# Optimization experiments

Measured on AMD Instinct MI355X. Metric: run time of the kernel, lower is better.

## Reference

```python
import jax, jax.numpy as jnp
import numpy as np

B, T, E, H, L, V = 2, 1024, 1024, 16, 4, 32000
HS = E // H
EPS = 1e-5


def layernorm(x, g, b):
    m = jnp.mean(x, axis=-1, keepdims=True)
    v = jnp.mean((x - m) ** 2, axis=-1, keepdims=True)
    return (x - m) * jax.lax.rsqrt(v + EPS) * g + b


def setup_inputs() -> dict:
    key = jax.random.key(0)
    ks = jax.random.split(key, 20)
    s = 0.02
    inp = {
        "ids": jax.random.randint(ks[0], (B, T), 0, V, dtype=jnp.int32),
        "emb": jax.random.normal(ks[1], (V, E), jnp.float32) * s,
        "pos": jax.random.normal(ks[2], (T, E), jnp.float32) * s,
        "wq": jax.random.normal(ks[3], (L, E, E), jnp.float32) * s,
        "bq": jnp.zeros((L, E), jnp.float32),
        "wk": jax.random.normal(ks[4], (L, E, E), jnp.float32) * s,
        "bk": jnp.zeros((L, E), jnp.float32),
        "wv": jax.random.normal(ks[5], (L, E, E), jnp.float32) * s,
        "bv": jnp.zeros((L, E), jnp.float32),
        "w1": jax.random.normal(ks[6], (L, E, 4 * E), jnp.float32) * s,
        "b1": jnp.zeros((L, 4 * E), jnp.float32),
        "w2": jax.random.normal(ks[7], (L, 4 * E, E), jnp.float32) * s,
        "b2": jnp.zeros((L, E), jnp.float32),
        "ln1_g": jnp.ones((L, E), jnp.float32),
        "ln1_b": jnp.zeros((L, E), jnp.float32),
        "ln2_g": jnp.ones((L, E), jnp.float32),
        "ln2_b": jnp.zeros((L, E), jnp.float32),
        "proj_w": jax.random.normal(ks[8], (E, V), jnp.float32) * s,
        "proj_b": jnp.zeros((V,), jnp.float32),
    }
    return inp


def reference(ids, emb, pos, wq, bq, wk, bk, wv, bv, w1, b1, w2, b2,
              ln1_g, ln1_b, ln2_g, ln2_b, proj_w, proj_b):
    x = emb[ids] + pos[:ids.shape[-1]]  # [B,T,E]
    scale = 1.0 / (E ** 0.5)  # NOTE: original divides by embed_size**0.5
    causal = jnp.tril(jnp.ones((T, T), dtype=bool))
    for l in range(L):
        h = layernorm(x, ln1_g[l], ln1_b[l])
        q = (h @ wq[l] + bq[l]).reshape(B, T, H, HS).transpose(0, 2, 1, 3)
        k = (h @ wk[l] + bk[l]).reshape(B, T, H, HS).transpose(0, 2, 1, 3)
        v = (h @ wv[l] + bv[l]).reshape(B, T, H, HS).transpose(0, 2, 1, 3)
        scores = jnp.einsum('bhqd,bhkd->bhqk', q, k) * scale
        scores = jnp.where(causal, scores, -jnp.inf)
        attn = jax.nn.softmax(scores, axis=-1)
        o = jnp.einsum('bhqk,bhkd->bhqd', attn, v)
        o = o.transpose(0, 2, 1, 3).reshape(B, T, E)
        x = x + o
        h2 = layernorm(x, ln2_g[l], ln2_b[l])
        ff = jax.nn.gelu(h2 @ w1[l] + b1[l], approximate=False) @ w2[l] + b2[l]
        x = x + ff  # Dropout(0.2) in eval mode = identity
    logits = x @ proj_w + proj_b  # [B,T,V]
    return logits
```

## Files before the change

kernel.cpp:

```cpp
#include <hip/hip_runtime.h>
#include <hip/hip_bf16.h>
#include <cstdint>

#define B_    2
#define T_    1024
#define E_    1024
#define H_    16
#define HS_   64
#define L_    4
#define V_    32000
#define FF_   4096
#define BT_   2048
#define EPS_  1e-5f
#define SCALE_ 0.03125f

typedef __bf16 bf16;
typedef bf16  bf16x4 __attribute__((ext_vector_type(4)));
typedef bf16  bf16x8 __attribute__((ext_vector_type(8)));
typedef float f32x4  __attribute__((ext_vector_type(4)));

#define GL2LDS(gp, lp) __builtin_amdgcn_global_load_lds( \
    (const __attribute__((address_space(1))) void*)(gp), \
    (__attribute__((address_space(3))) void*)(lp), 16, 0, 0)

__global__ __launch_bounds__(256) void embed_kernel(
    const int* __restrict__ ids, const float* __restrict__ emb,
    const float* __restrict__ pos, float* __restrict__ x)
{
  int bt = blockIdx.x;
  int t  = bt & (T_ - 1);
  int id = ids[bt];
  f32x4 e = *(const f32x4*)(emb + (size_t)id * E_ + threadIdx.x * 4);
  f32x4 p = *(const f32x4*)(pos + (size_t)t  * E_ + threadIdx.x * 4);
  *(f32x4*)(x + (size_t)bt * E_ + threadIdx.x * 4) = e + p;
}

__device__ __forceinline__ float wred_sum(float v) {
#pragma unroll
  for (int o = 32; o; o >>= 1) v += __shfl_xor(v, o, 64);
  return v;
}

__global__ __launch_bounds__(256) void ln_kernel(
    const float* __restrict__ x, const float* __restrict__ g,
    const float* __restrict__ b, bf16* __restrict__ h)
{
  int row = blockIdx.x, tid = threadIdx.x;
  f32x4 v = *(const f32x4*)(x + (size_t)row * E_ + tid * 4);
  float s  = v[0] + v[1] + v[2] + v[3];
  float sq = v[0]*v[0] + v[1]*v[1] + v[2]*v[2] + v[3]*v[3];
  s  = wred_sum(s);
  sq = wred_sum(sq);
  __shared__ float rs[4], rq[4];
  int w = tid >> 6, lane = tid & 63;
  if (lane == 0) { rs[w] = s; rq[w] = sq; }
  __syncthreads();
  float S = rs[0] + rs[1] + rs[2] + rs[3];
  float Q = rq[0] + rq[1] + rq[2] + rq[3];
  float mean = S * (1.0f / E_);
  float var  = Q * (1.0f / E_) - mean * mean;
  float rstd = rsqrtf(fmaxf(var, 0.0f) + EPS_);
  f32x4 gv = *(const f32x4*)(g + tid * 4);
  f32x4 bv = *(const f32x4*)(b + tid * 4);
  f32x4 o = (v - mean) * rstd * gv + bv;
  bf16x4 ob = { (bf16)o[0], (bf16)o[1], (bf16)o[2], (bf16)o[3] };
  *(bf16x4*)(h + (size_t)row * E_ + tid * 4) = ob;
}

__global__ __launch_bounds__(256) void convw_kernel(
    const float* __restrict__ W0, const float* __restrict__ W1, const float* __restrict__ W2,
    bf16* __restrict__ O0, bf16* __restrict__ O1, bf16* __restrict__ O2,
    int K, int ldW)
{
  int z = blockIdx.z;
  const float* W = (z == 0) ? W0 : (z == 1) ? W1 : W2;
  bf16*        O = (z == 0) ? O0 : (z == 1) ? O1 : O2;
  __shared__ float tl[32][33];
  int n0 = blockIdx.x * 32, k0 = blockIdx.y * 32;
  int c = threadIdx.x & 31, r = threadIdx.x >> 5;
#pragma unroll
  for (int p = 0; p < 4; ++p)
    tl[r + p * 8][c] = W[(size_t)(k0 + r + p * 8) * ldW + n0 + c];
  __syncthreads();
#pragma unroll
  for (int p = 0; p < 4; ++p)
    O[(size_t)(n0 + r + p * 8) * K + k0 + c] = (bf16)tl[c][r + p * 8];
}

template <int ACT, int MODE>
__global__ __launch_bounds__(256) void gemm_bf16(
    const bf16* __restrict__ A,
    const bf16* __restrict__ B0, const bf16* __restrict__ B1, const bf16* __restrict__ B2,
    const float* __restrict__ bi0, const float* __restrict__ bi1, const float* __restrict__ bi2,
    bf16* __restrict__ Cb0, bf16* __restrict__ Cb1, bf16* __restrict__ Cb2,
    float* __restrict__ Cf, const float* __restrict__ R,
    int K, int ldc, int LDK)
{
  int z = blockIdx.z;
  const bf16*  Bm = (MODE == 3) ? B0 : (z == 0) ? B0 : (z == 1) ? B1 : B2;
  const float* bi = (z == 0) ? bi0 : (z == 1) ? bi1 : bi2;
  bf16*        Cb = (z == 0) ? Cb0 : (z == 1) ? Cb1 : Cb2;
  int koff = (MODE == 3) ? z * K : 0;

  int nb  = (int)(gridDim.x * gridDim.y);
  int lin = blockIdx.x + gridDim.x * blockIdx.y;
  int per = nb >> 3;
  int b   = (lin & 7) * per + (lin >> 3);
  int mi  = b & 15;
  int ni  = b >> 4;

  __shared__ __align__(16) char lds[2][16384];

  int tid = threadIdx.x;
  int lane = tid & 63, wid = tid >> 6;
  int wm = (wid >> 1) * 64, wn = (wid & 1) * 64;
  int fr = lane & 15, fb = lane >> 4;

  const bf16* Asrc = A  + (size_t)(mi * 128) * LDK + koff;
  const bf16* Bsrc = Bm + (size_t)(ni * 128) * LDK + koff;

  int NT = K >> 5;

#define STAGE(buf, kk)                                                          \
  {                                                                             \
    _Pragma("unroll")                                                           \
    for (int is = 0; is < 2; ++is) {                                            \
      int rl = is * 64 + (tid >> 2);                                            \
      int key = (rl >> 1) & 3;                                                  \
      int ck  = ((tid & 3) ^ key) * 8;                                          \
      GL2LDS(Asrc + (size_t)rl * LDK + (kk) + ck,                               \
             lds[buf] + is * 4096 + tid * 16);                                  \
      GL2LDS(Bsrc + (size_t)rl * LDK + (kk) + ck,                               \
             lds[buf] + 8192 + is * 4096 + tid * 16);                           \
    }                                                                           \
  }

  f32x4 acc[4][4];
#pragma unroll
  for (int i = 0; i < 4; ++i)
#pragma unroll
    for (int j = 0; j < 4; ++j) acc[i][j] = (f32x4){0.f, 0.f, 0.f, 0.f};

  STAGE(0, 0);
  int cur = 0;

  for (int t = 0; t < NT; ++t) {
    __syncthreads();
    if (t + 1 < NT) STAGE(cur ^ 1, (t + 1) << 5);

    const char* Ab = lds[cur];
    const char* Bb = lds[cur] + 8192;
    bf16x8 af[4], bfr[4];
#pragma unroll
    for (int i = 0; i < 4; ++i) {
      int rl = wm + i * 16 + fr;
      af[i] = *(const bf16x8*)(Ab + rl * 64 + ((fb ^ ((rl >> 1) & 3)) * 16));
    }
#pragma unroll
    for (int j = 0; j < 4; ++j) {
      int rl = wn + j * 16 + fr;
      bfr[j] = *(const bf16x8*)(Bb + rl * 64 + ((fb ^ ((rl >> 1) & 3)) * 16));
    }
#pragma unroll
    for (int i = 0; i < 4; ++i)
#pragma unroll
      for (int j = 0; j < 4; ++j)
        acc[i][j] = __builtin_amdgcn_mfma_f32_16x16x32_bf16(af[i], bfr[j], acc[i][j], 0, 0, 0);
    cur ^= 1;
  }
#undef STAGE

#pragma unroll
  for (int i = 0; i < 4; ++i) {
#pragma unroll
    for (int j = 0; j < 4; ++j) {
      int gc = ni * 128 + wn + j * 16 + fr;
      float bv = (MODE == 3) ? 0.f : bi[gc];
#pragma unroll
      for (int r = 0; r < 4; ++r) {
        int gr = mi * 128 + wm + i * 16 + fb * 4 + r;
        float vv = acc[i][j][r] + bv;
        if (ACT == 1) vv = 0.5f * vv * (1.0f + erff(vv * 0.70710678118654752f));
        if (MODE == 2) {
          float nv = vv + R[(size_t)gr * ldc + gc];
          Cf[(size_t)gr * ldc + gc] = nv;
          Cb[(size_t)gr * ldc + gc] = (bf16)nv;
        } else if (MODE == 1) {
          Cb[(size_t)gr * ldc + gc] = (bf16)vv;
        } else if (MODE == 3) {
          Cf[(size_t)(z * BT_ + gr) * ldc + gc] = vv;
        }
      }
    }
  }
}

__global__ __launch_bounds__(256) void combine_kernel(
    const float* __restrict__ p, const float* __restrict__ bi,
    float* __restrict__ x, bf16* __restrict__ xb)
{
  int row = blockIdx.x, tid = threadIdx.x;
  size_t off = (size_t)row * E_ + tid * 4;
  f32x4 a = *(const f32x4*)(p + off);
  f32x4 c = *(const f32x4*)(p + (size_t)BT_ * E_ + off);
  f32x4 bv = *(const f32x4*)(bi + tid * 4);
  f32x4 xv = *(const f32x4*)(x + off);
  f32x4 nv = xv + a + c + bv;
  *(f32x4*)(x + off) = nv;
  bf16x4 ob = { (bf16)nv[0], (bf16)nv[1], (bf16)nv[2], (bf16)nv[3] };
  *(bf16x4*)(xb + off) = ob;
}

__global__ __launch_bounds__(512, 2) void gemm256_kernel(
    const bf16* __restrict__ A, const bf16* __restrict__ Bm,
    const float* __restrict__ bi, float* __restrict__ C, int K, int N)
{
  int nwg = (int)gridDim.x;
  int per = nwg >> 3;
  int bid = (int)blockIdx.x;
  int tl  = (bid & 7) * per + (bid >> 3);
  int mi  = tl & 7, ni = tl >> 3;

  __shared__ __align__(16) char lds[2][65536];

  int tid = threadIdx.x;
  int lane = tid & 63, wid = tid >> 6;
  int wr = wid >> 2, wc = wid & 3;
  int fr = lane & 15, fb = lane >> 4;

  const bf16* Asrc = A  + (size_t)(mi * 256) * K;
  const bf16* Bsrc = Bm + (size_t)(ni * 256) * K;

  int NT = K >> 6;

#define STAGE256(buf, kk)                                                  \
  { _Pragma("unroll")                                                      \
    for (int h = 0; h < 2; ++h) {                                          \
      _Pragma("unroll")                                                    \
      for (int is = 0; is < 2; ++is) {                                     \
        int ri  = is * 64 + (tid >> 3);                                    \
        int ck  = (tid & 7) ^ (ri & 7);                                    \
        int row = h * 128 + ri;                                            \
        GL2LDS(Asrc + (size_t)row * K + (kk) + ck * 8,                     \
               lds[buf] + h * 16384 + is * 8192 + tid * 16);               \
        GL2LDS(Bsrc + (size_t)row * K + (kk) + ck * 8,                     \
               lds[buf] + 32768 + h * 16384 + is * 8192 + tid * 16);       \
      }                                                                    \
    } }

  f32x4 acc[8][4];
#pragma unroll
  for (int i = 0; i < 8; ++i)
#pragma unroll
    for (int j = 0; j < 4; ++j) acc[i][j] = (f32x4){0.f, 0.f, 0.f, 0.f};

  STAGE256(0, 0);

  for (int t = 0; t < NT; ++t) {
    int buf = t & 1;
    if (t + 1 < NT) {
      STAGE256(buf ^ 1, (t + 1) << 6);
      asm volatile("s_waitcnt vmcnt(8)" ::: "memory");
    } else {
      asm volatile("s_waitcnt vmcnt(0)" ::: "memory");
    }
    __builtin_amdgcn_s_barrier();
    asm volatile("" ::: "memory");

    const char* Ab = lds[buf];
    const char* Bb = lds[buf] + 32768;

    bf16x8 bfr[4][2];
#pragma unroll
    for (int n2 = 0; n2 < 4; ++n2) {
      int row = wc * 64 + n2 * 16 + fr;
#pragma unroll
      for (int ks = 0; ks < 2; ++ks)
        bfr[n2][ks] = *(const bf16x8*)(Bb + (row >> 7) * 16384 + (row & 127) * 128
                                          + ((((ks * 4 + fb) ^ (fr & 7))) << 4));
    }
#pragma unroll
    for (int q = 0; q < 4; ++q) {
      bf16x8 af[2][2];
#pragma unroll
      for (int m2 = 0; m2 < 2; ++m2) {
        int ri = (q * 2 + m2) * 16 + fr;
#pragma unroll
        for (int ks = 0; ks < 2; ++ks)
          af[m2][ks] = *(const bf16x8*)(Ab + wr * 16384 + ri * 128
                                           + ((((ks * 4 + fb) ^ (fr & 7))) << 4));
      }
      __builtin_amdgcn_s_setprio(1);
#pragma unroll
      for (int m2 = 0; m2 < 2; ++m2)
#pragma unroll
        for (int n2 = 0; n2 < 4; ++n2)
#pragma unroll
          for (int ks = 0; ks < 2; ++ks)
            acc[q * 2 + m2][n2] = __builtin_amdgcn_mfma_f32_16x16x32_bf16(
                af[m2][ks], bfr[n2][ks], acc[q * 2 + m2][n2], 0, 0, 0);
      __builtin_amdgcn_s_setprio(0);
    }
    asm volatile("" ::: "memory");
    __builtin_amdgcn_s_barrier();
  }
#undef STAGE256

#pragma unroll
  for (int i = 0; i < 8; ++i) {
#pragma unroll
    for (int j = 0; j < 4; ++j) {
      int gc = ni * 256 + wc * 64 + j * 16 + fr;
      float bv = bi[gc];
#pragma unroll
      for (int r = 0; r < 4; ++r) {
        int gr = mi * 256 + wr * 128 + i * 16 + fb * 4 + r;
        C[(size_t)gr * N + gc] = acc[i][j][r] + bv;
      }
    }
  }
}

__global__ __launch_bounds__(256) void attn_kernel(
    const bf16* __restrict__ q, const bf16* __restrict__ k,
    const bf16* __restrict__ v, float* __restrict__ x)
{
  __shared__ __align__(16) char Ks[8192];
  __shared__ __align__(16) char Vs[8192];
  __shared__ __align__(16) char Ps[8192];

  int tid = threadIdx.x, lane = tid & 63, w = tid >> 6;
  int qt = blockIdx.x, bh = blockIdx.y;
  int b = bh >> 4, h = bh & 15;
  size_t hoff = (size_t)b * T_ * E_ + h * HS_;
  int fr = lane & 15, fb = lane >> 4;

  bf16x8 qa[2];
  {
    const bf16* qp = q + hoff + (size_t)(qt * 64 + w * 16 + fr) * E_ + fb * 8;
    qa[0] = *(const bf16x8*)qp;
    qa[1] = *(const bf16x8*)(qp + 32);
  }

  f32x4 O[4];
  float m_[4], l_[4];
#pragma unroll
  for (int i = 0; i < 4; ++i) { O[i] = (f32x4){0.f,0.f,0.f,0.f}; m_[i] = -1e30f; l_[i] = 0.f; }

  for (int kt = 0; kt <= qt; ++kt) {
    __syncthreads();
    {
      const bf16* kbase = k + hoff + (size_t)(kt * 64) * E_;
#pragma unroll
      for (int is = 0; is < 2; ++is) {
        int c = is * 32 + (tid >> 3);
        int key = ((c & 7) ^ (c >> 3)) & 7;
        GL2LDS(kbase + (size_t)c * E_ + (((tid & 7) ^ key) * 8),
               Ks + is * 4096 + tid * 16);
      }
    }
#pragma unroll
    for (int p = 0; p < 2; ++p) {
      int row = tid >> 2;
      int d0 = (tid & 3) * 8 + p * 32;
      bf16x8 vv = *(const bf16x8*)(v + hoff + (size_t)(kt * 64 + row) * E_ + d0);
#pragma unroll
      for (int e = 0; e < 8; ++e) {
        int d = d0 + e;
        int key = ((d & 7) ^ (d >> 3)) & 7;
        *(bf16*)(Vs + d * 128 + ((row * 2) ^ (key << 4))) = vv[e];
      }
    }
    __syncthreads();

    f32x4 s[4];
#pragma unroll
    for (int jc = 0; jc < 4; ++jc) {
      s[jc] = (f32x4){0.f, 0.f, 0.f, 0.f};
#pragma unroll
      for (int kc = 0; kc < 2; ++kc) {
        int c = jc * 16 + fr;
        int key = ((c & 7) ^ (c >> 3)) & 7;
        bf16x8 kf = *(const bf16x8*)(Ks + c * 128 + ((kc * 64 + fb * 16) ^ (key << 4)));
        s[jc] = __builtin_amdgcn_mfma_f32_16x16x32_bf16(qa[kc], kf, s[jc], 0, 0, 0);
      }
    }

    char* pbase = Ps + w * 2048;
#pragma unroll
    for (int r = 0; r < 4; ++r) {
      float s0 = s[0][r] * SCALE_, s1 = s[1][r] * SCALE_;
      float s2 = s[2][r] * SCALE_, s3 = s[3][r] * SCALE_;
      int qrow = qt * 64 + w * 16 + fb * 4 + r;
      if (kt == qt) {
        int kc0 = kt * 64 + fr;
        if (kc0      > qrow) s0 = -1e30f;
        if (kc0 + 16 > qrow) s1 = -1e30f;
        if (kc0 + 32 > qrow) s2 = -1e30f;
        if (kc0 + 48 > qrow) s3 = -1e30f;
      }
      float mx = fmaxf(fmaxf(s0, s1), fmaxf(s2, s3));
      mx = fmaxf(mx, __shfl_xor(mx, 1, 16));
      mx = fmaxf(mx, __shfl_xor(mx, 2, 16));
      mx = fmaxf(mx, __shfl_xor(mx, 4, 16));
      mx = fmaxf(mx, __shfl_xor(mx, 8, 16));
      float mnew = fmaxf(m_[r], mx);
      float p0 = __expf(s0 - mnew), p1 = __expf(s1 - mnew);
      float p2 = __expf(s2 - mnew), p3 = __expf(s3 - mnew);
      float rs = p0 + p1 + p2 + p3;
      rs += __shfl_xor(rs, 1, 16);
      rs += __shfl_xor(rs, 2, 16);
      rs += __shfl_xor(rs, 4, 16);
      rs += __shfl_xor(rs, 8, 16);
      float scl = __expf(m_[r] - mnew);
      l_[r] = l_[r] * scl + rs;
      m_[r] = mnew;
#pragma unroll
      for (int jd = 0; jd < 4; ++jd) O[jd][r] *= scl;
      int key2 = (r << 4) ^ (fb << 5);
      char* pr_ = pbase + (fb * 4 + r) * 128;
      *(bf16*)(pr_ + (( 0 + fr * 2) ^ key2)) = (bf16)p0;
      *(bf16*)(pr_ + ((32 + fr * 2) ^ key2)) = (bf16)p1;
      *(bf16*)(pr_ + ((64 + fr * 2) ^ key2)) = (bf16)p2;
      *(bf16*)(pr_ + ((96 + fr * 2) ^ key2)) = (bf16)p3;
    }

#pragma unroll
    for (int kc = 0; kc < 2; ++kc) {
      int key2 = ((fr & 3) << 4) ^ ((fr >> 2) << 5);
      bf16x8 pa = *(const bf16x8*)(pbase + fr * 128 + ((kc * 64 + fb * 16) ^ key2));
#pragma unroll
      for (int jd = 0; jd < 4; ++jd) {
        int d = jd * 16 + fr;
        int key = ((d & 7) ^ (d >> 3)) & 7;
        bf16x8 vf = *(const bf16x8*)(Vs + d * 128 + ((kc * 64 + fb * 16) ^ (key << 4)));
        O[jd] = __builtin_amdgcn_mfma_f32_16x16x32_bf16(pa, vf, O[jd], 0, 0, 0);
      }
    }
  }

#pragma unroll
  for (int r = 0; r < 4; ++r) {
    float inv = 1.0f / l_[r];
    float* xp = x + hoff + (size_t)(qt * 64 + w * 16 + fb * 4 + r) * E_;
#pragma unroll
    for (int jd = 0; jd < 4; ++jd) {
      int d = jd * 16 + fr;
      xp[d] += O[jd][r] * inv;
    }
  }
}

extern "C" void kernel_launch(void* const* d_in, const int* in_sizes, int n_in,
                              void* d_out, int out_size, void* d_ws, size_t ws_size,
                              hipStream_t stream)
{
  const int*   ids  = (const int*)  d_in[0];
  const float* emb  = (const float*)d_in[1];
  const float* pos  = (const float*)d_in[2];
  const float* wq   = (const float*)d_in[3];
  const float* bq   = (const float*)d_in[4];
  const float* wk   = (const float*)d_in[5];
  const float* bk   = (const float*)d_in[6];
  const float* wv   = (const float*)d_in[7];
  const float* bv   = (const float*)d_in[8];
  const float* w1   = (const float*)d_in[9];
  const float* b1   = (const float*)d_in[10];
  const float* w2   = (const float*)d_in[11];
  const float* b2   = (const float*)d_in[12];
  const float* ln1g = (const float*)d_in[13];
  const float* ln1b = (const float*)d_in[14];
  const float* ln2g = (const float*)d_in[15];
  const float* ln2b = (const float*)d_in[16];
  const float* pw   = (const float*)d_in[17];
  const float* pb   = (const float*)d_in[18];
  float* out = (float*)d_out;

  if (ws_size < (size_t)17 * 1024 * 1024 * 4) return;
  float* ws = (float*)d_ws;
  float* x   = ws;
  bf16*  hb  = (bf16*)(ws + (size_t) 2 * 1024 * 1024);
  bf16*  qb  = (bf16*)(ws + (size_t) 3 * 1024 * 1024);
  bf16*  kb  = (bf16*)(ws + (size_t) 4 * 1024 * 1024);
  bf16*  vb  = (bf16*)(ws + (size_t) 5 * 1024 * 1024);
  bf16*  ffb = (bf16*)(ws + (size_t) 6 * 1024 * 1024);
  float* fp  = ws + (size_t)2 * 1024 * 1024;
  bf16*  lwb = (bf16*)(ws + (size_t)10 * 1024 * 1024);
  bf16*  xb  = (bf16*)(ws + (size_t)16 * 1024 * 1024);
  bf16*  pwb = (bf16*)ws;
  bf16*  wqt = lwb;
  bf16*  wkt = lwb + (size_t)1 * 1024 * 1024;
  bf16*  wvt = lwb + (size_t)2 * 1024 * 1024;
  bf16*  w1t = lwb + (size_t)3 * 1024 * 1024;
  bf16*  w2t = lwb + (size_t)7 * 1024 * 1024;

  embed_kernel<<<BT_, 256, 0, stream>>>(ids, emb, pos, x);

  for (int l = 0; l < L_; ++l) {
    const size_t lEE = (size_t)l * E_ * E_;
    const size_t lEF = (size_t)l * E_ * FF_;

    convw_kernel<<<dim3(E_/32, E_/32, 3), 256, 0, stream>>>(
        wq + lEE, wk + lEE, wv + lEE, wqt, wkt, wvt, E_, E_);
    convw_kernel<<<dim3(FF_/32, E_/32, 1), 256, 0, stream>>>(
        w1 + lEF, nullptr, nullptr, w1t, nullptr, nullptr, E_, FF_);
    convw_kernel<<<dim3(E_/32, FF_/32, 1), 256, 0, stream>>>(
        w2 + lEF, nullptr, nullptr, w2t, nullptr, nullptr, FF_, E_);

    ln_kernel<<<BT_, 256, 0, stream>>>(x, ln1g + l*E_, ln1b + l*E_, hb);

    gemm_bf16<0,1><<<dim3(16, E_/128, 3), 256, 0, stream>>>(
        hb, wqt, wkt, wvt, bq + l*E_, bk + l*E_, bv + l*E_,
        qb, kb, vb, nullptr, nullptr, E_, E_, E_);

    attn_kernel<<<dim3(T_/64, B_*H_), 256, 0, stream>>>(qb, kb, vb, x);

    ln_kernel<<<BT_, 256, 0, stream>>>(x, ln2g + l*E_, ln2b + l*E_, hb);

    gemm_bf16<1,1><<<dim3(16, FF_/128, 1), 256, 0, stream>>>(
        hb, w1t, nullptr, nullptr, b1 + (size_t)l*FF_, nullptr, nullptr,
        ffb, nullptr, nullptr, nullptr, nullptr, E_, FF_, E_);

    gemm_bf16<0,3><<<dim3(16, E_/128, 2), 256, 0, stream>>>(
        ffb, w2t, nullptr, nullptr, nullptr, nullptr, nullptr,
        nullptr, nullptr, nullptr, fp, nullptr, FF_/2, E_, FF_);
    combine_kernel<<<BT_, 256, 0, stream>>>(fp, b2 + l*E_, x, xb);
  }

  convw_kernel<<<dim3(V_/32, E_/32, 1), 256, 0, stream>>>(
      pw, nullptr, nullptr, pwb, nullptr, nullptr, E_, V_);
  gemm256_kernel<<<(V_/256) * 8, 512, 0, stream>>>(
      xb, pwb, pb, out, E_, V_);
}
```

Before: 860.6 us.

## Merge weight conversions, fuse FFN2 residual epilogue, shrink projection GEMM K-tile

The three per-layer weight transpose/convert launches become one combined launch. The split-K FFN2 GEMM plus its separate combine kernel is replaced by a 128x64-tile GEMM that adds bias and residual in its epilogue and writes both the fp32 and bf16 copies of x. This removes a partial-sum round trip and a launch, at the cost of 256 blocks over full K. The vocab projection GEMM drops its K-tile from 64 to 32, halving LDS so occupancy can rise to 4 blocks, with a new swizzle and wait count.

After: 1.755 ms. +103.9%, slower.

```diff
diff --git a/kernel.cpp b/kernel.cpp
--- a/kernel.cpp
+++ b/kernel.cpp
@@ -68,18 +68,48 @@
 }
 
 __global__ __launch_bounds__(256) void convw_kernel(
-    const float* __restrict__ W0, const float* __restrict__ W1, const float* __restrict__ W2,
-    bf16* __restrict__ O0, bf16* __restrict__ O1, bf16* __restrict__ O2,
-    int K, int ldW)
-{
-  int z = blockIdx.z;
-  const float* W = (z == 0) ? W0 : (z == 1) ? W1 : W2;
-  bf16*        O = (z == 0) ? O0 : (z == 1) ? O1 : O2;
+    const float* __restrict__ W0, bf16* __restrict__ O0, int K, int ldW)
+{
   __shared__ float tl[32][33];
   int n0 = blockIdx.x * 32, k0 = blockIdx.y * 32;
   int c = threadIdx.x & 31, r = threadIdx.x >> 5;
 #pragma unroll
   for (int p = 0; p < 4; ++p)
+    tl[r + p * 8][c] = W0[(size_t)(k0 + r + p * 8) * ldW + n0 + c];
+  __syncthreads();
+#pragma unroll
+  for (int p = 0; p < 4; ++p)
+    O0[(size_t)(n0 + r + p * 8) * K + k0 + c] = (bf16)tl[c][r + p * 8];
+}
+
+__global__ __launch_bounds__(256) void convw_all(
+    const float* __restrict__ wq, const float* __restrict__ wk,
+    const float* __restrict__ wv, const float* __restrict__ w1,
+    const float* __restrict__ w2,
+    bf16* __restrict__ oq, bf16* __restrict__ ok, bf16* __restrict__ ov,
+    bf16* __restrict__ o1, bf16* __restrict__ o2)
+{
+  int bid = blockIdx.x;
+  const float* W; bf16* O; int K, ldW, nx, ny;
+  if (bid < 3072) {
+    int z = bid >> 10, rem = bid & 1023;
+    W = (z == 0) ? wq : (z == 1) ? wk : wv;
+    O = (z == 0) ? oq : (z == 1) ? ok : ov;
+    K = 1024; ldW = 1024; nx = rem & 31; ny = rem >> 5;
+  } else if (bid < 7168) {
+    int idx = bid - 3072;
+    W = w1; O = o1; K = 1024; ldW = 4096;
+    nx = idx & 127; ny = idx >> 7;
+  } else {
+    int idx = bid - 7168;
+    W = w2; O = o2; K = 4096; ldW = 1024;
+    nx = idx & 31; ny = idx >> 5;
+  }
+  __shared__ float tl[32][33];
+  int n0 = nx * 32, k0 = ny * 32;
+  int c = threadIdx.x & 31, r = threadIdx.x >> 5;
+#pragma unroll
+  for (int p = 0; p < 4; ++p)
     tl[r + p * 8][c] = W[(size_t)(k0 + r + p * 8) * ldW + n0 + c];
   __syncthreads();
 #pragma unroll
@@ -87,20 +117,18 @@
     O[(size_t)(n0 + r + p * 8) * K + k0 + c] = (bf16)tl[c][r + p * 8];
 }
 
-template <int ACT, int MODE>
+template <int ACT>
 __global__ __launch_bounds__(256) void gemm_bf16(
     const bf16* __restrict__ A,
     const bf16* __restrict__ B0, const bf16* __restrict__ B1, const bf16* __restrict__ B2,
     const float* __restrict__ bi0, const float* __restrict__ bi1, const float* __restrict__ bi2,
     bf16* __restrict__ Cb0, bf16* __restrict__ Cb1, bf16* __restrict__ Cb2,
-    float* __restrict__ Cf, const float* __restrict__ R,
-    int K, int ldc, int LDK)
+    int K, int ldc)
 {
   int z = blockIdx.z;
-  const bf16*  Bm = (MODE == 3) ? B0 : (z == 0) ? B0 : (z == 1) ? B1 : B2;
+  const bf16*  Bm = (z == 0) ? B0 : (z == 1) ? B1 : B2;
   const float* bi = (z == 0) ? bi0 : (z == 1) ? bi1 : bi2;
   bf16*        Cb = (z == 0) ? Cb0 : (z == 1) ? Cb1 : Cb2;
-  int koff = (MODE == 3) ? z * K : 0;
 
   int nb  = (int)(gridDim.x * gridDim.y);
   int lin = blockIdx.x + gridDim.x * blockIdx.y;
@@ -116,8 +144,8 @@
   int wm = (wid >> 1) * 64, wn = (wid & 1) * 64;
   int fr = lane & 15, fb = lane >> 4;
 
-  const bf16* Asrc = A  + (size_t)(mi * 128) * LDK + koff;
-  const bf16* Bsrc = Bm + (size_t)(ni * 128) * LDK + koff;
+  const bf16* Asrc = A  + (size_t)(mi * 128) * K;
+  const bf16* Bsrc = Bm + (size_t)(ni * 128) * K;
 
   int NT = K >> 5;
 
@@ -128,9 +156,9 @@
       int rl = is * 64 + (tid >> 2);                                            \
       int key = (rl >> 1) & 3;                                                  \
       int ck  = ((tid & 3) ^ key) * 8;                                          \
-      GL2LDS(Asrc + (size_t)rl * LDK + (kk) + ck,                               \
+      GL2LDS(Asrc + (size_t)rl * K + (kk) + ck,                                 \
              lds[buf] + is * 4096 + tid * 16);                                  \
-      GL2LDS(Bsrc + (size_t)rl * LDK + (kk) + ck,                               \
+      GL2LDS(Bsrc + (size_t)rl * K + (kk) + ck,                                 \
              lds[buf] + 8192 + is * 4096 + tid * 16);                           \
     }                                                                           \
   }
@@ -175,43 +203,112 @@
 #pragma unroll
     for (int j = 0; j < 4; ++j) {
       int gc = ni * 128 + wn + j * 16 + fr;
-      float bv = (MODE == 3) ? 0.f : bi[gc];
+      float bv = bi[gc];
 #pragma unroll
       for (int r = 0; r < 4; ++r) {
         int gr = mi * 128 + wm + i * 16 + fb * 4 + r;
         float vv = acc[i][j][r] + bv;
         if (ACT == 1) vv = 0.5f * vv * (1.0f + erff(vv * 0.70710678118654752f));
-        if (MODE == 2) {
-          float nv = vv + R[(size_t)gr * ldc + gc];
-          Cf[(size_t)gr * ldc + gc] = nv;
-          Cb[(size_t)gr * ldc + gc] = (bf16)nv;
-        } else if (MODE == 1) {
-          Cb[(size_t)gr * ldc + gc] = (bf16)vv;
-        } else if (MODE == 3) {
-          Cf[(size_t)(z * BT_ + gr) * ldc + gc] = vv;
-        }
-      }
-    }
-  }
-}
-
-__global__ __launch_bounds__(256) void combine_kernel(
-    const float* __restrict__ p, const float* __restrict__ bi,
-    float* __restrict__ x, bf16* __restrict__ xb)
-{
-  int row = blockIdx.x, tid = threadIdx.x;
-  size_t off = (size_t)row * E_ + tid * 4;
-  f32x4 a = *(const f32x4*)(p + off);
-  f32x4 c = *(const f32x4*)(p + (size_t)BT_ * E_ + off);
-  f32x4 bv = *(const f32x4*)(bi + tid * 4);
-  f32x4 xv = *(const f32x4*)(x + off);
-  f32x4 nv = xv + a + c + bv;
-  *(f32x4*)(x + off) = nv;
-  bf16x4 ob = { (bf16)nv[0], (bf16)nv[1], (bf16)nv[2], (bf16)nv[3] };
-  *(bf16x4*)(xb + off) = ob;
-}
-
-__global__ __launch_bounds__(512, 2) void gemm256_kernel(
+        Cb[(size_t)gr * ldc + gc] = (bf16)vv;
+      }
+    }
+  }
+}
+
+__global__ __launch_bounds__(256) void ffn2_kernel(
+    const bf16* __restrict__ A, const bf16* __restrict__ Bm,
+    const float* __restrict__ bi, float* __restrict__ x,
+    bf16* __restrict__ xb, int K)
+{
+  int nb  = (int)(gridDim.x * gridDim.y);
+  int lin = blockIdx.x + gridDim.x * blockIdx.y;
+  int per = nb >> 3;
+  int b   = (lin & 7) * per + (lin >> 3);
+  int mi  = b & 15, ni = b >> 4;
+
+  __shared__ __align__(16) char lds[2][12288];
+
+  int tid = threadIdx.x;
+  int lane = tid & 63, wid = tid >> 6;
+  int wm = (wid >> 1) * 64, wn = (wid & 1) * 32;
+  int fr = lane & 15, fb = lane >> 4;
+
+  const bf16* Asrc = A  + (size_t)(mi * 128) * K;
+  const bf16* Bsrc = Bm + (size_t)(ni * 64) * K;
+
+  int NT = K >> 5;
+
+#define STAGEF(buf, kk)                                                         \
+  {                                                                             \
+    _Pragma("unroll")                                                           \
+    for (int is = 0; is < 2; ++is) {                                            \
+      int c   = is * 256 + tid;                                                 \
+      int row = c >> 2;                                                         \
+      int ck  = ((c & 3) ^ ((row >> 1) & 3)) * 8;                               \
+      GL2LDS(Asrc + (size_t)row * K + (kk) + ck, lds[buf] + c * 16);            \
+    }                                                                           \
+    {                                                                           \
+      int c   = tid;                                                            \
+      int row = c >> 2;                                                         \
+      int ck  = ((c & 3) ^ ((row >> 1) & 3)) * 8;                               \
+      GL2LDS(Bsrc + (size_t)row * K + (kk) + ck, lds[buf] + 8192 + c * 16);     \
+    }                                                                           \
+  }
+
+  f32x4 acc[4][2];
+#pragma unroll
+  for (int i = 0; i < 4; ++i)
+#pragma unroll
+    for (int j = 0; j < 2; ++j) acc[i][j] = (f32x4){0.f, 0.f, 0.f, 0.f};
+
+  STAGEF(0, 0);
+  int cur = 0;
+
+  for (int t = 0; t < NT; ++t) {
+    __syncthreads();
+    if (t + 1 < NT) STAGEF(cur ^ 1, (t + 1) << 5);
+
+    const char* Ab = lds[cur];
+    const char* Bb = lds[cur] + 8192;
+    bf16x8 af[4], bfr[2];
+#pragma unroll
+    for (int i = 0; i < 4; ++i) {
+      int rl = wm + i * 16 + fr;
+      af[i] = *(const bf16x8*)(Ab + rl * 64 + ((fb ^ ((rl >> 1) & 3)) * 16));
+    }
+#pragma unroll
+    for (int j = 0; j < 2; ++j) {
+      int rl = wn + j * 16 + fr;
+      bfr[j] = *(const bf16x8*)(Bb + rl * 64 + ((fb ^ ((rl >> 1) & 3)) * 16));
+    }
+#pragma unroll
+    for (int i = 0; i < 4; ++i)
+#pragma unroll
+      for (int j = 0; j < 2; ++j)
+        acc[i][j] = __builtin_amdgcn_mfma_f32_16x16x32_bf16(af[i], bfr[j], acc[i][j], 0, 0, 0);
+    cur ^= 1;
+  }
+#undef STAGEF
+
+#pragma unroll
+  for (int i = 0; i < 4; ++i) {
+#pragma unroll
+    for (int j = 0; j < 2; ++j) {
+      int gc = ni * 64 + wn + j * 16 + fr;
+      float bv = bi[gc];
+#pragma unroll
+      for (int r = 0; r < 4; ++r) {
+        int gr = mi * 128 + wm + i * 16 + fb * 4 + r;
+        size_t off = (size_t)gr * E_ + gc;
+        float nv = acc[i][j][r] + bv + x[off];
+        x[off]  = nv;
+        xb[off] = (bf16)nv;
+      }
+    }
+  }
+}
+
+__global__ __launch_bounds__(512, 4) void gemm256_kernel(
     const bf16* __restrict__ A, const bf16* __restrict__ Bm,
     const float* __restrict__ bi, float* __restrict__ C, int K, int N)
 {
@@ -221,7 +318,7 @@
   int tl  = (bid & 7) * per + (bid >> 3);
   int mi  = tl & 7, ni = tl >> 3;
 
-  __shared__ __align__(16) char lds[2][65536];
+  __shared__ __align__(16) char lds[2][32768];
 
   int tid = threadIdx.x;
   int lane = tid & 63, wid = tid >> 6;
@@ -231,21 +328,18 @@
   const bf16* Asrc = A  + (size_t)(mi * 256) * K;
   const bf16* Bsrc = Bm + (size_t)(ni * 256) * K;
 
-  int NT = K >> 6;
+  int NT = K >> 5;
 
 #define STAGE256(buf, kk)                                                  \
   { _Pragma("unroll")                                                      \
-    for (int h = 0; h < 2; ++h) {                                          \
-      _Pragma("unroll")                                                    \
-      for (int is = 0; is < 2; ++is) {                                     \
-        int ri  = is * 64 + (tid >> 3);                                    \
-        int ck  = (tid & 7) ^ (ri & 7);                                    \
-        int row = h * 128 + ri;                                            \
-        GL2LDS(Asrc + (size_t)row * K + (kk) + ck * 8,                     \
-               lds[buf] + h * 16384 + is * 8192 + tid * 16);               \
-        GL2LDS(Bsrc + (size_t)row * K + (kk) + ck * 8,                     \
-               lds[buf] + 32768 + h * 16384 + is * 8192 + tid * 16);       \
-      }                                                                    \
+    for (int is = 0; is < 2; ++is) {                                       \
+      int c   = is * 512 + tid;                                            \
+      int row = c >> 2;                                                    \
+      int ck  = ((c & 3) ^ ((row >> 1) & 3)) * 8;                          \
+      GL2LDS(Asrc + (size_t)row * K + (kk) + ck,                           \
+             lds[buf] + c * 16);                                           \
+      GL2LDS(Bsrc + (size_t)row * K + (kk) + ck,                           \
+             lds[buf] + 16384 + c * 16);                                   \
     } }
 
   f32x4 acc[8][4];
@@ -259,8 +353,8 @@
   for (int t = 0; t < NT; ++t) {
     int buf = t & 1;
     if (t + 1 < NT) {
-      STAGE256(buf ^ 1, (t + 1) << 6);
-      asm volatile("s_waitcnt vmcnt(8)" ::: "memory");
+      STAGE256(buf ^ 1, (t + 1) << 5);
+      asm volatile("s_waitcnt vmcnt(4)" ::: "memory");
     } else {
       asm volatile("s_waitcnt vmcnt(0)" ::: "memory");
     }
@@ -268,37 +362,29 @@
     asm volatile("" ::: "memory");
 
     const char* Ab = lds[buf];
-    const char* Bb = lds[buf] + 32768;
-
-    bf16x8 bfr[4][2];
+    const char* Bb = lds[buf] + 16384;
+
+    bf16x8 bfr[4];
 #pragma unroll
     for (int n2 = 0; n2 < 4; ++n2) {
       int row = wc * 64 + n2 * 16 + fr;
-#pragma unroll
-      for (int ks = 0; ks < 2; ++ks)
-        bfr[n2][ks] = *(const bf16x8*)(Bb + (row >> 7) * 16384 + (row & 127) * 128
-                                          + ((((ks * 4 + fb) ^ (fr & 7))) << 4));
+      bfr[n2] = *(const bf16x8*)(Bb + row * 64 + ((fb ^ ((row >> 1) & 3)) << 4));
     }
 #pragma unroll
     for (int q = 0; q < 4; ++q) {
-      bf16x8 af[2][2];
+      bf16x8 af[2];
 #pragma unroll
       for (int m2 = 0; m2 < 2; ++m2) {
-        int ri = (q * 2 + m2) * 16 + fr;
-#pragma unroll
-        for (int ks = 0; ks < 2; ++ks)
-          af[m2][ks] = *(const bf16x8*)(Ab + wr * 16384 + ri * 128
-                                           + ((((ks * 4 + fb) ^ (fr & 7))) << 4));
+        int row = wr * 128 + (q * 2 + m2) * 16 + fr;
+        af[m2] = *(const bf16x8*)(Ab + row * 64 + ((fb ^ ((row >> 1) & 3)) << 4));
       }
       __builtin_amdgcn_s_setprio(1);
 #pragma unroll
       for (int m2 = 0; m2 < 2; ++m2)
 #pragma unroll
         for (int n2 = 0; n2 < 4; ++n2)
-#pragma unroll
-          for (int ks = 0; ks < 2; ++ks)
-            acc[q * 2 + m2][n2] = __builtin_amdgcn_mfma_f32_16x16x32_bf16(
-                af[m2][ks], bfr[n2][ks], acc[q * 2 + m2][n2], 0, 0, 0);
+          acc[q * 2 + m2][n2] = __builtin_amdgcn_mfma_f32_16x16x32_bf16(
+              af[m2], bfr[n2], acc[q * 2 + m2][n2], 0, 0, 0);
       __builtin_amdgcn_s_setprio(0);
     }
     asm volatile("" ::: "memory");
@@ -484,7 +570,6 @@
   bf16*  kb  = (bf16*)(ws + (size_t) 4 * 1024 * 1024);
   bf16*  vb  = (bf16*)(ws + (size_t) 5 * 1024 * 1024);
   bf16*  ffb = (bf16*)(ws + (size_t) 6 * 1024 * 1024);
-  float* fp  = ws + (size_t)2 * 1024 * 1024;
   bf16*  lwb = (bf16*)(ws + (size_t)10 * 1024 * 1024);
   bf16*  xb  = (bf16*)(ws + (size_t)16 * 1024 * 1024);
   bf16*  pwb = (bf16*)ws;
@@ -500,35 +585,29 @@
     const size_t lEE = (size_t)l * E_ * E_;
     const size_t lEF = (size_t)l * E_ * FF_;
 
-    convw_kernel<<<dim3(E_/32, E_/32, 3), 256, 0, stream>>>(
-        wq + lEE, wk + lEE, wv + lEE, wqt, wkt, wvt, E_, E_);
-    convw_kernel<<<dim3(FF_/32, E_/32, 1), 256, 0, stream>>>(
-        w1 + lEF, nullptr, nullptr, w1t, nullptr, nullptr, E_, FF_);
-    convw_kernel<<<dim3(E_/32, FF_/32, 1), 256, 0, stream>>>(
-        w2 + lEF, nullptr, nullptr, w2t, nullptr, nullptr, FF_, E_);
+    convw_all<<<11264, 256, 0, stream>>>(
+        wq + lEE, wk + lEE, wv + lEE, w1 + lEF, w2 + lEF,
+        wqt, wkt, wvt, w1t, w2t);
 
     ln_kernel<<<BT_, 256, 0, stream>>>(x, ln1g + l*E_, ln1b + l*E_, hb);
 
-    gemm_bf16<0,1><<<dim3(16, E_/128, 3), 256, 0, stream>>>(
+    gemm_bf16<0><<<dim3(16, E_/128, 3), 256, 0, stream>>>(
         hb, wqt, wkt, wvt, bq + l*E_, bk + l*E_, bv + l*E_,
-        qb, kb, vb, nullptr, nullptr, E_, E_, E_);
+        qb, kb, vb, E_, E_);
 
     attn_kernel<<<dim3(T_/64, B_*H_), 256, 0, stream>>>(qb, kb, vb, x);
 
     ln_kernel<<<BT_, 256, 0, stream>>>(x, ln2g + l*E_, ln2b + l*E_, hb);
 
-    gemm_bf16<1,1><<<dim3(16, FF_/128, 1), 256, 0, stream>>>(
+    gemm_bf16<1><<<dim3(16, FF_/128, 1), 256, 0, stream>>>(
         hb, w1t, nullptr, nullptr, b1 + (size_t)l*FF_, nullptr, nullptr,
-        ffb, nullptr, nullptr, nullptr, nullptr, E_, FF_, E_);
-
-    gemm_bf16<0,3><<<dim3(16, E_/128, 2), 256, 0, stream>>>(
-        ffb, w2t, nullptr, nullptr, nullptr, nullptr, nullptr,
-        nullptr, nullptr, nullptr, fp, nullptr, FF_/2, E_, FF_);
-    combine_kernel<<<BT_, 256, 0, stream>>>(fp, b2 + l*E_, x, xb);
-  }
-
-  convw_kernel<<<dim3(V_/32, E_/32, 1), 256, 0, stream>>>(
-      pw, nullptr, nullptr, pwb, nullptr, nullptr, E_, V_);
+        ffb, nullptr, nullptr, E_, FF_);
+
+    ffn2_kernel<<<dim3(16, 16), 256, 0, stream>>>(
+        ffb, w2t, b2 + l*E_, x, xb, FF_);
+  }
+
+  convw_kernel<<<dim3(V_/32, E_/32), 256, 0, stream>>>(pw, pwb, E_, V_);
   gemm256_kernel<<<(V_/256) * 8, 512, 0, stream>>>(
       xb, pwb, pb, out, E_, V_);
 }
```
